# Kernel tuning notes

Hardware: AMD Instinct MI355X
Metric: run time of the kernel (lower is better)

Reference implementation:

```python
import jax, jax.numpy as jnp
import numpy as np

N = 50000   # total nodes
E = 100000  # total edges
F = 64      # input node features
H = 128     # hidden_dim
HEADS = 4
B = 64      # number of graphs in the batch
S = 512     # num_stations
LC = 8      # num_line_colors


def setup_inputs() -> dict:
    key = jax.random.key(0)
    ks = jax.random.split(key, 40)
    w = lambda i, shape: (jax.random.normal(ks[i], shape, jnp.float32) * 0.02)
    inp = {
        'node_features': jax.random.normal(ks[0], (N, F), jnp.float32),
        'edge_index': jax.random.randint(ks[1], (2, E), 0, N),
        'batch': jnp.sort(jax.random.randint(ks[2], (N,), 0, B)),
        # initial projection F -> H
        'Wp': w(3, (F, H)), 'bp': w(4, (H,)),
        # TransformerConv 1: in H, out H, heads HEADS (concat)
        'Wq1': w(5, (H, HEADS * H)), 'bq1': w(6, (HEADS * H,)),
        'Wk1': w(7, (H, HEADS * H)), 'bk1': w(8, (HEADS * H,)),
        'Wv1': w(9, (H, HEADS * H)), 'bv1': w(10, (HEADS * H,)),
        'Ws1': w(11, (H, HEADS * H)), 'bs1': w(12, (HEADS * H,)),
        # TransformerConv 2: in HEADS*H, out H, heads 1
        'Wq2': w(13, (HEADS * H, H)), 'bq2': w(14, (H,)),
        'Wk2': w(15, (HEADS * H, H)), 'bk2': w(16, (H,)),
        'Wv2': w(17, (HEADS * H, H)), 'bv2': w(18, (H,)),
        'Ws2': w(19, (HEADS * H, H)), 'bs2': w(20, (H,)),
        # output heads
        'crW': w(21, (H, 1)),  'crb': w(22, (1,)),
        'hlW': w(23, (H, 4)),  'hlb': w(24, (4,)),
        'mtW': w(25, (H, 3)),  'mtb': w(26, (3,)),
        'p1W': w(27, (H, S)),  'p1b': w(28, (S,)),
        'p2W': w(29, (H, S)),  'p2b': w(30, (S,)),
        'dtW': w(31, (H, S)),  'dtb': w(32, (S,)),
        'slW': w(33, (H, LC)), 'slb': w(34, (LC,)),
    }
    return inp


def transformer_conv(x, src, dst, Wq, bq, Wk, bk, Wv, bv, Ws, bs, heads, out_ch):
    # PyG TransformerConv (beta=False, concat=True, root_weight=True):
    #   alpha_ij = softmax_j( (W_q x_i) . (W_k x_j) / sqrt(d) ) over in-edges of i
    #   out_i    = sum_j alpha_ij * (W_v x_j)  (concat heads) + W_skip x_i
    n = x.shape[0]
    q = (x @ Wq + bq).reshape(n, heads, out_ch)
    k = (x @ Wk + bk).reshape(n, heads, out_ch)
    v = (x @ Wv + bv).reshape(n, heads, out_ch)
    scores = jnp.sum(q[dst] * k[src], axis=-1) / jnp.sqrt(jnp.float32(out_ch))  # [E,heads]
    m = jax.ops.segment_max(scores, dst, num_segments=n)                        # per-target max
    e = jnp.exp(scores - m[dst])
    denom = jax.ops.segment_sum(e, dst, num_segments=n)
    alpha = e / (denom[dst] + 1e-16)                                            # [E,heads]
    out = jax.ops.segment_sum(alpha[:, :, None] * v[src], dst, num_segments=n)  # [N,heads,out]
    return out.reshape(n, heads * out_ch) + (x @ Ws + bs)


def reference(node_features, edge_index, batch, Wp, bp,
              Wq1, bq1, Wk1, bk1, Wv1, bv1, Ws1, bs1,
              Wq2, bq2, Wk2, bk2, Wv2, bv2, Ws2, bs2,
              crW, crb, hlW, hlb, mtW, mtb, p1W, p1b, p2W, p2b, dtW, dtb, slW, slb):
    src, dst = edge_index[0], edge_index[1]
    h = jax.nn.relu(node_features @ Wp + bp)
    h = jax.nn.relu(transformer_conv(h, src, dst, Wq1, bq1, Wk1, bk1, Wv1, bv1, Ws1, bs1, HEADS, H))
    h = jax.nn.relu(transformer_conv(h, src, dst, Wq2, bq2, Wk2, bk2, Wv2, bv2, Ws2, bs2, 1, H))
    # global mean pool over graphs
    counts = jax.ops.segment_sum(jnp.ones((h.shape[0],), h.dtype), batch, num_segments=B)
    g = jax.ops.segment_sum(h, batch, num_segments=B) / jnp.maximum(counts, 1.0)[:, None]  # [B,H]
    value = g @ crW + crb
    return (value,
            g @ hlW + hlb,
            g @ mtW + mtb,
            g @ p1W + p1b,
            g @ p2W + p2b,
            g @ dtW + dtb,
            g @ slW + slb)
```

## Files before the change

kernel.cpp:

```cpp
#include <hip/hip_runtime.h>
#include <hip/hip_bf16.h>

#define NN 50000
#define EE 100000
#define FF 64
#define HH 128
#define HEADS 4
#define BB 64
#define SS 512
#define LCC 8

__device__ __forceinline__ float b2f(ushort u) {
    return __uint_as_float(((unsigned)u) << 16);
}
__device__ __forceinline__ ushort f2b(float f) {
    unsigned u = __float_as_uint(f);
    unsigned r = (u + 0x7FFFu + ((u >> 16) & 1u)) >> 16;
    return (ushort)r;
}
__device__ __forceinline__ uint f2b_pk(float a, float b) {
    __hip_bfloat162 h = __float22bfloat162_rn(make_float2(a, b));
    return *reinterpret_cast<uint*>(&h);
}

__device__ __forceinline__ uint f2fp8x4(float a, float b, float c, float d) {
    int r = __builtin_amdgcn_cvt_pk_fp8_f32(a, b, 0, false);
    r = __builtin_amdgcn_cvt_pk_fp8_f32(c, d, r, true);
    return (uint)r;
}
__device__ __forceinline__ float fp8lo(ushort u) { return __builtin_amdgcn_cvt_f32_fp8((int)u, 0); }
__device__ __forceinline__ float fp8hi(ushort u) { return __builtin_amdgcn_cvt_f32_fp8((int)u, 1); }

typedef __attribute__((ext_vector_type(4))) float f32x4;
typedef __attribute__((ext_vector_type(8))) short s16x8;
typedef __attribute__((ext_vector_type(4))) uint u32x4;

__device__ __forceinline__ void glls16(const ushort* g, ushort* l) {
    __builtin_amdgcn_global_load_lds((const __attribute__((address_space(1))) void*)g,
                                     (__attribute__((address_space(3))) void*)l, 16, 0, 0);
}

#define BM 128
#define BN 128
#define BK 64
#define EST 68

__global__ __launch_bounds__(256) void gemm_bf16(
    const ushort* __restrict__ A, const ushort* __restrict__ Bt,
    const float* __restrict__ bias,
    ushort* __restrict__ C1, int ld1,
    ushort* __restrict__ C2b, int mode,
    int M, int K, int relu, int gx, int gy)
{
    __shared__ __align__(16) ushort Sm[2 * BM * BK];
    ushort* As = Sm;
    ushort* Bs = Sm + BM * BK;

    const int bid  = blockIdx.x;
    const int xcd  = bid & 7;
    const int slot = bid >> 3;
    const int bx   = slot % gx;
    const int by   = xcd + 8 * (slot / gx);
    if (by >= gy) return;
    const int m0 = by * BM;
    const int n0 = bx * BN;

    const int t = threadIdx.x;
    const int lane = t & 63;
    const int wave = t >> 6;
    const int wm = (wave & 1) * 64;
    const int wn = (wave >> 1) * 64;
    const int lrow = lane & 15;
    const int g    = lane >> 4;

    const int wbase = n0 + wn;
    float bj[4];
#pragma unroll
    for (int j = 0; j < 4; ++j) bj[j] = bias[wbase + j * 16 + lrow];

    const int srow = (wave << 5) + (lane >> 3);
    const int scs  = lane & 7;

    const ushort* ga[4];
    const ushort* gb[4];
#pragma unroll
    for (int p = 0; p < 4; ++p) {
        const int row = srow + (p << 3);
        const int l   = scs ^ (row & 7);
        ga[p] = A + (size_t)min(m0 + row, M - 1) * K + (l << 3);
        gb[p] = Bt + (size_t)(n0 + row) * K + (l << 3);
    }
    const int ldsoff = (wave << 11);

    f32x4 acc[4][4];
#pragma unroll
    for (int i = 0; i < 4; ++i)
#pragma unroll
        for (int j = 0; j < 4; ++j)
            acc[i][j] = (f32x4){bj[j], bj[j], bj[j], bj[j]};

    for (int k0 = 0; k0 < K; k0 += BK) {
#pragma unroll
        for (int p = 0; p < 4; ++p) glls16(ga[p] + k0, As + ldsoff + (p << 9));
#pragma unroll
        for (int p = 0; p < 4; ++p) glls16(gb[p] + k0, Bs + ldsoff + (p << 9));
        __syncthreads();

#pragma unroll
        for (int kk = 0; kk < 2; ++kk) {
            s16x8 af[4], bf[4];
#pragma unroll
            for (int i = 0; i < 4; ++i) {
                const int R = wm + i * 16 + lrow;
                const int c = ((kk << 2) + g) ^ (R & 7);
                af[i] = *(const s16x8*)&As[(R << 6) + (c << 3)];
            }
#pragma unroll
            for (int j = 0; j < 4; ++j) {
                const int R = wn + j * 16 + lrow;
                const int c = ((kk << 2) + g) ^ (R & 7);
                bf[j] = *(const s16x8*)&Bs[(R << 6) + (c << 3)];
            }
#pragma unroll
            for (int i = 0; i < 4; ++i)
#pragma unroll
                for (int j = 0; j < 4; ++j)
                    acc[i][j] = __builtin_amdgcn_mfma_f32_16x16x32_bf16(af[i], bf[j], acc[i][j], 0, 0, 0);
        }
        __syncthreads();
    }

    float* Es = (float*)Sm + wave * (16 * EST);

    bool e8 = false;
    ushort* Cw = C1; int ldw = ld1; int cb = wbase;
    unsigned char* Cw8 = nullptr;
    if (mode == 1) {
        if (wbase >= 512) {
            e8 = true;
            const int u = wbase - 512;
            const int h = u >> 8;
            cb = u & 255;
            Cw8 = (unsigned char*)C2b + (size_t)h * NN * 256;
            ldw = 256;
        }
    } else if (mode == 2) {
        if (wbase < 128) { ldw = 128; }
        else {
            e8 = true;
            Cw8 = (unsigned char*)C2b;
            ldw = 384;
            cb = wbase - 128;
        }
    }

    const int rbase = (lane >> 4) * 4;
    const int rrow  = lane >> 2;
    const int rcol  = (lane & 3) << 4;

#pragma unroll
    for (int i = 0; i < 4; ++i) {
#pragma unroll
        for (int j = 0; j < 4; ++j)
#pragma unroll
            for (int r = 0; r < 4; ++r) {
                float v = acc[i][j][r];
                if (relu) v = fmaxf(v, 0.f);
                Es[(rbase + r) * EST + j * 16 + lrow] = v;
            }
        const int gm = m0 + wm + i * 16 + rrow;
        if (gm < M) {
            const float* srcp = Es + rrow * EST + rcol;
            f32x4 f0 = *(const f32x4*)(srcp + 0);
            f32x4 f1 = *(const f32x4*)(srcp + 4);
            f32x4 f2 = *(const f32x4*)(srcp + 8);
            f32x4 f3 = *(const f32x4*)(srcp + 12);
            if (!e8) {
                u32x4 o0, o1;
                o0[0] = f2b_pk(f0[0], f0[1]); o0[1] = f2b_pk(f0[2], f0[3]);
                o0[2] = f2b_pk(f1[0], f1[1]); o0[3] = f2b_pk(f1[2], f1[3]);
                o1[0] = f2b_pk(f2[0], f2[1]); o1[1] = f2b_pk(f2[2], f2[3]);
                o1[2] = f2b_pk(f3[0], f3[1]); o1[3] = f2b_pk(f3[2], f3[3]);
                ushort* dst = Cw + (size_t)gm * ldw + cb + rcol;
                *(u32x4*)(dst + 0) = o0;
                *(u32x4*)(dst + 8) = o1;
            } else {
                u32x4 o;
                o[0] = f2fp8x4(f0[0], f0[1], f0[2], f0[3]);
                o[1] = f2fp8x4(f1[0], f1[1], f1[2], f1[3]);
                o[2] = f2fp8x4(f2[0], f2[1], f2[2], f2[3]);
                o[3] = f2fp8x4(f3[0], f3[1], f3[2], f3[3]);
                *(u32x4*)(Cw8 + (size_t)gm * ldw + cb + rcol) = o;
            }
        }
    }
}

#define F1OFF  8192
#define F2OFF  204800
#define WTOTAL 466944
#define BTOT   2048
#define MWORK  (HEADS * 128 * 128 + HEADS * 128)

__global__ void prep_kernel(
    const float* __restrict__ Wp,
    const float* __restrict__ Wq1, const float* __restrict__ Wk1,
    const float* __restrict__ Wv1, const float* __restrict__ Ws1,
    const float* __restrict__ Wq2, const float* __restrict__ Wk2,
    const float* __restrict__ Wv2, const float* __restrict__ Ws2,
    const float* __restrict__ bs1, const float* __restrict__ bq1,
    const float* __restrict__ bv1, const float* __restrict__ bs2,
    const float* __restrict__ bq2, const float* __restrict__ bk2, const float* __restrict__ bv2,
    ushort* __restrict__ wt, float* __restrict__ bb)
{
    int t = blockIdx.x * 256 + threadIdx.x;
    if (t < WTOTAL) {
        float v;
        if (t < F1OFF) {
            int n = t >> 6, k = t & 63;
            v = Wp[k * 128 + n];
        } else if (t < F2OFF) {
            int u = t - F1OFF;
            int n = u >> 7, k = u & 127;
            if (n < 512) v = Ws1[k * 512 + n];
            else {
                int r = n - 512;
                int h = r >> 8, c = r & 255;
                if (c < 128) return;
                v = Wv1[k * 512 + h * 128 + (c - 128)] * 16.0f;
            }
        } else {
            int u = t - F2OFF;
            int n = u >> 9, k = u & 511;
            if (n < 128) v = Ws2[k * 128 + n];
            else {
                int r = n - 128;
                const float* W = (r < 128) ? Wq2 : (r < 256) ? Wk2 : Wv2;
                v = W[k * 128 + (r & 127)] * 16.0f;
            }
        }
        wt[t] = f2b(v);
    } else if (t < WTOTAL + BTOT) {
        int u = t - WTOTAL;
        float v;
        if (u < 512) v = bs1[u];
        else if (u < 1536) {
            int r = u - 512;
            int h = r >> 8, c = r & 255;
            if (c < 128) return;
            v = bv1[h * 128 + (c - 128)] * 16.0f;
        } else {
            int c = u - 1536;
            v = (c < 128) ? bs2[c]
              : (c < 256) ? bq2[c - 128] * 16.0f
              : (c < 384) ? bk2[c - 256] * 16.0f : bv2[c - 384] * 16.0f;
        }
        bb[u] = v;
    } else if (t < WTOTAL + BTOT + MWORK) {
        int m = t - (WTOTAL + BTOT);
        if (m < HEADS * 128 * 128) {
            int h = m >> 14;
            int rem = m & 16383;
            int b = rem >> 7, a = rem & 127;
            const float* wq = Wq1 + a * 512 + h * 128;
            const float* wk = Wk1 + b * 512 + h * 128;
            float acc = 0.f;
#pragma unroll 8
            for (int d = 0; d < 128; ++d) acc += wq[d] * wk[d];
            wt[F1OFF + (size_t)(512 + h * 256 + b) * 128 + a] = f2b(acc * 16.0f);
        } else {
            int u = m - HEADS * 128 * 128;
            int h = u >> 7, b = u & 127;
            const float* wk = Wk1 + b * 512 + h * 128;
            const float* bq = bq1 + h * 128;
            float acc = 0.f;
#pragma unroll 8
            for (int d = 0; d < 128; ++d) acc += wk[d] * bq[d];
            bb[512 + h * 256 + b] = acc * 16.0f;
        }
    }
}

__global__ void f32_to_bf16_kernel(const float4* __restrict__ in, uint2* __restrict__ out, int n4)
{
    int i = blockIdx.x * 256 + threadIdx.x;
    if (i >= n4) return;
    float4 v = in[i];
    uint2 o;
    o.x = f2b_pk(v.x, v.y);
    o.y = f2b_pk(v.z, v.w);
    out[i] = o;
}

__global__ void fill_kernel(unsigned* __restrict__ p, unsigned v, int n) {
    int i = blockIdx.x * blockDim.x + threadIdx.x;
    if (i < n) p[i] = v;
}

__global__ void hist_kernel(const int* __restrict__ dst, int* __restrict__ cnt, int E) {
    int e = blockIdx.x * 256 + threadIdx.x;
    if (e < E) atomicAdd(&cnt[dst[e]], 1);
}

#define SCAN_B 1024
__global__ void scan_bsum_kernel(const int* __restrict__ cnt, int* __restrict__ bsum, int n) {
    __shared__ int sd[256];
    int tid = threadIdx.x;
    int base = blockIdx.x * SCAN_B + tid * 4;
    int s = 0;
#pragma unroll
    for (int j = 0; j < 4; ++j) if (base + j < n) s += cnt[base + j];
    sd[tid] = s;
    __syncthreads();
    for (int off = 128; off > 0; off >>= 1) {
        if (tid < off) sd[tid] += sd[tid + off];
        __syncthreads();
    }
    if (tid == 0) bsum[blockIdx.x] = sd[0];
}

__global__ void scan_final_kernel(const int* __restrict__ cnt, const int* __restrict__ bsum,
                                  int* __restrict__ rowptr, int* __restrict__ cursor, int n) {
    __shared__ int sd[256];
    __shared__ int sb[256];
    int tid = threadIdx.x;
    sb[tid] = (tid < blockIdx.x) ? bsum[tid] : 0;
    __syncthreads();
    for (int off = 128; off > 0; off >>= 1) {
        if (tid < off) sb[tid] += sb[tid + off];
        __syncthreads();
    }
    const int bbase = sb[0];

    int base = blockIdx.x * SCAN_B + tid * 4;
    int v[4]; int s = 0;
#pragma unroll
    for (int j = 0; j < 4; ++j) { v[j] = (base + j < n) ? cnt[base + j] : 0; s += v[j]; }
    sd[tid] = s;
    __syncthreads();
    for (int off = 1; off < 256; off <<= 1) {
        int t2 = (tid >= off) ? sd[tid - off] : 0;
        __syncthreads();
        sd[tid] += t2;
        __syncthreads();
    }
    int acc = bbase + sd[tid] - s;
#pragma unroll
    for (int j = 0; j < 4; ++j) {
        if (base + j < n) cursor[base + j] = acc;
        acc += v[j];
        if (base + j < n) rowptr[base + j + 1] = acc;
    }
    if (blockIdx.x == 0 && tid == 0) rowptr[0] = 0;
}

__global__ void bucket_kernel(const int* __restrict__ src, const int* __restrict__ dst,
                              int* __restrict__ cursor, int* __restrict__ srcs, int E) {
    int e = blockIdx.x * 256 + threadIdx.x;
    if (e >= E) return;
    int p = atomicAdd(&cursor[dst[e]], 1);
    srcs[p] = src[e];
}

__global__ __launch_bounds__(256) void gather4_kernel(
    const unsigned char* __restrict__ Qb, const ushort* __restrict__ Kb,
    const int* __restrict__ rowptr, const int* __restrict__ srcs,
    ushort* __restrict__ io, float scale, int n)
{
    int i = blockIdx.x * 4 + (threadIdx.x >> 6);
    int lane = threadIdx.x & 63;
    if (i >= n) return;
    const ushort* Qu = (const ushort*)Qb;
    const uint* Ku = (const uint*)Kb;

    float q0[4], q1[4];
#pragma unroll
    for (int h = 0; h < 4; ++h) {
        ushort qv = Qu[((size_t)h * NN + i) * 128 + lane];
        q0[h] = fp8lo(qv); q1[h] = fp8hi(qv);
    }
    int p0 = rowptr[i], p1 = rowptr[i + 1];
    float den[4] = {0.f, 0.f, 0.f, 0.f};
    float o0[4] = {0.f, 0.f, 0.f, 0.f};
    float o1[4] = {0.f, 0.f, 0.f, 0.f};
    int p = p0;
    for (; p + 2 <= p1; p += 2) {
        int s0 = srcs[p], s1 = srcs[p + 1];
        uint kva = Ku[(size_t)s0 * 64 + lane];
        uint kvb = Ku[(size_t)s1 * 64 + lane];
        ushort vva[4], vvb[4];
#pragma unroll
        for (int h = 0; h < 4; ++h) vva[h] = Qu[((size_t)h * NN + s0) * 128 + 64 + lane];
#pragma unroll
        for (int h = 0; h < 4; ++h) vvb[h] = Qu[((size_t)h * NN + s1) * 128 + 64 + lane];
        float ka0 = b2f((ushort)kva), ka1 = b2f((ushort)(kva >> 16));
        float kb0 = b2f((ushort)kvb), kb1 = b2f((ushort)(kvb >> 16));
        float da[4], db[4];
#pragma unroll
        for (int h = 0; h < 4; ++h) {
            da[h] = q0[h] * ka0 + q1[h] * ka1;
            db[h] = q0[h] * kb0 + q1[h] * kb1;
        }
#pragma unroll
        for (int off = 32; off > 0; off >>= 1) {
#pragma unroll
            for (int h = 0; h < 4; ++h) {
                da[h] += __shfl_xor(da[h], off, 64);
                db[h] += __shfl_xor(db[h], off, 64);
            }
        }
#pragma unroll
        for (int h = 0; h < 4; ++h) {
            float ea = __expf(da[h] * scale);
            float eb = __expf(db[h] * scale);
            den[h] += ea + eb;
            o0[h] += ea * fp8lo(vva[h]) + eb * fp8lo(vvb[h]);
            o1[h] += ea * fp8hi(vva[h]) + eb * fp8hi(vvb[h]);
        }
    }
    if (p < p1) {
        int s = srcs[p];
        uint kv = Ku[(size_t)s * 64 + lane];
        ushort vv[4];
#pragma unroll
        for (int h = 0; h < 4; ++h) vv[h] = Qu[((size_t)h * NN + s) * 128 + 64 + lane];
        float k0 = b2f((ushort)kv), k1 = b2f((ushort)(kv >> 16));
        float d[4];
#pragma unroll
        for (int h = 0; h < 4; ++h) d[h] = q0[h] * k0 + q1[h] * k1;
#pragma unroll
        for (int off = 32; off > 0; off >>= 1) {
#pragma unroll
            for (int h = 0; h < 4; ++h) d[h] += __shfl_xor(d[h], off, 64);
        }
#pragma unroll
        for (int h = 0; h < 4; ++h) {
            float e = __expf(d[h] * scale);
            den[h] += e;
            o0[h] += e * fp8lo(vv[h]);
            o1[h] += e * fp8hi(vv[h]);
        }
    }
#pragma unroll
    for (int h = 0; h < 4; ++h) {
        uint sk = ((const uint*)io)[(size_t)i * 256 + h * 64 + lane];
        float inv = 0.0625f / (den[h] + 1e-16f);
        float r0 = fmaxf(b2f((ushort)sk) + o0[h] * inv, 0.f);
        float r1 = fmaxf(b2f((ushort)(sk >> 16)) + o1[h] * inv, 0.f);
        ((uint*)io)[(size_t)i * 256 + h * 64 + lane] = f2b_pk(r0, r1);
    }
}

__global__ __launch_bounds__(256) void edge_gather_kernel(
    const unsigned char* __restrict__ qkv,
    const int* __restrict__ rowptr, const int* __restrict__ srcs,
    const ushort* __restrict__ skip,
    ushort* __restrict__ outp, float scale, int n)
{
    int i = blockIdx.x * 4 + (threadIdx.x >> 6);
    int lane = threadIdx.x & 63;
    if (i >= n) return;
    const ushort* Qu = (const ushort*)qkv;

    uint sk = ((const uint*)skip)[(size_t)i * 64 + lane];
    ushort qv = Qu[(size_t)i * 192 + lane];
    float q0 = fp8lo(qv), q1 = fp8hi(qv);
    int p0 = rowptr[i], p1 = rowptr[i + 1];
    float den = 0.f, o0 = 0.f, o1 = 0.f;
    int p = p0;
    for (; p + 2 <= p1; p += 2) {
        int s0 = srcs[p], s1 = srcs[p + 1];
        const ushort* kr0 = Qu + (size_t)s0 * 192 + 64;
        const ushort* kr1 = Qu + (size_t)s1 * 192 + 64;
        ushort kv0 = kr0[lane], vv0 = kr0[lane + 64];
        ushort kv1 = kr1[lane], vv1 = kr1[lane + 64];
        float d0 = q0 * fp8lo(kv0) + q1 * fp8hi(kv0);
        float d1 = q0 * fp8lo(kv1) + q1 * fp8hi(kv1);
#pragma unroll
        for (int off = 32; off > 0; off >>= 1) {
            d0 += __shfl_xor(d0, off, 64);
            d1 += __shfl_xor(d1, off, 64);
        }
        float e0 = __expf(d0 * scale), e1 = __expf(d1 * scale);
        den += e0 + e1;
        o0 += e0 * fp8lo(vv0) + e1 * fp8lo(vv1);
        o1 += e0 * fp8hi(vv0) + e1 * fp8hi(vv1);
    }
    if (p < p1) {
        int s = srcs[p];
        const ushort* kr = Qu + (size_t)s * 192 + 64;
        ushort kv = kr[lane], vv = kr[lane + 64];
        float d = q0 * fp8lo(kv) + q1 * fp8hi(kv);
#pragma unroll
        for (int off = 32; off > 0; off >>= 1) d += __shfl_xor(d, off, 64);
        float e = __expf(d * scale);
        den += e;
        o0 += e * fp8lo(vv);
        o1 += e * fp8hi(vv);
    }
    float inv = 0.0625f / (den + 1e-16f);
    float r0 = b2f((ushort)sk) + o0 * inv;
    float r1 = b2f((ushort)(sk >> 16)) + o1 * inv;
    ((uint*)outp)[(size_t)i * 64 + lane] = f2b_pk(r0, r1);
}

__global__ __launch_bounds__(256) void pool_kernel(
    const ushort* __restrict__ h, const int* __restrict__ batch,
    float* __restrict__ gsum, float* __restrict__ cnt, int n)
{
    int wave = threadIdx.x >> 6, lane = threadIdx.x & 63;
    int start = blockIdx.x * 256 + wave * 64;
    int end = min(start + 64, n);
    if (start >= end) return;
    int cur = batch[start];
    float a0 = 0.f, a1 = 0.f;
    int run = 0;
    for (int node = start; node < end; ++node) {
        int g = batch[node];
        if (g != cur) {
            atomicAdd(&gsum[cur * HH + 2 * lane], a0);
            atomicAdd(&gsum[cur * HH + 2 * lane + 1], a1);
            if (lane == 0) atomicAdd(&cnt[cur], (float)run);
            cur = g; a0 = a1 = 0.f; run = 0;
        }
        uint x = ((const uint*)h)[(size_t)node * 64 + lane];
        a0 += fmaxf(b2f((ushort)x), 0.f);
        a1 += fmaxf(b2f((ushort)(x >> 16)), 0.f);
        ++run;
    }
    atomicAdd(&gsum[cur * HH + 2 * lane], a0);
    atomicAdd(&gsum[cur * HH + 2 * lane + 1], a1);
    if (lane == 0) atomicAdd(&cnt[cur], (float)run);
}

__global__ void pool_fin_kernel(const float* __restrict__ gsum,
                                const float* __restrict__ cnt, float* __restrict__ g)
{
    int i = blockIdx.x * blockDim.x + threadIdx.x;
    if (i < BB * HH) g[i] = gsum[i] / fmaxf(cnt[i / HH], 1.0f);
}

__global__ void out_heads_kernel(
    const float* __restrict__ g,
    const float* __restrict__ w0, const float* __restrict__ b0,
    const float* __restrict__ w1, const float* __restrict__ b1,
    const float* __restrict__ w2, const float* __restrict__ b2,
    const float* __restrict__ w3, const float* __restrict__ b3,
    const float* __restrict__ w4, const float* __restrict__ b4,
    const float* __restrict__ w5, const float* __restrict__ b5,
    const float* __restrict__ w6, const float* __restrict__ b6,
    float* __restrict__ out, int total)
{
    int t = blockIdx.x * blockDim.x + threadIdx.x;
    if (t >= total) return;
    const float* W; const float* bias; int cols; int local;
    if      (t < 64)    { W = w0; bias = b0; cols = 1;   local = t; }
    else if (t < 320)   { W = w1; bias = b1; cols = 4;   local = t - 64; }
    else if (t < 512)   { W = w2; bias = b2; cols = 3;   local = t - 320; }
    else if (t < 33280) { W = w3; bias = b3; cols = SS;  local = t - 512; }
    else if (t < 66048) { W = w4; bias = b4; cols = SS;  local = t - 33280; }
    else if (t < 98816) { W = w5; bias = b5; cols = SS;  local = t - 66048; }
    else                { W = w6; bias = b6; cols = LCC; local = t - 98816; }
    int b = local / cols, c = local % cols;
    const float* gr = g + b * HH;
    float acc = bias[c];
#pragma unroll 8
    for (int i = 0; i < HH; ++i) acc += gr[i] * W[i * cols + c];
    out[t] = acc;
}

extern "C" void kernel_launch(void* const* d_in, const int* in_sizes, int n_in,
                              void* d_out, int out_size, void* d_ws, size_t ws_size,
                              hipStream_t stream)
{
    (void)in_sizes; (void)n_in; (void)out_size; (void)ws_size;

    const float* nf   = (const float*)d_in[0];
    const int*   ei   = (const int*)d_in[1];
    const int*   src  = ei;
    const int*   dst  = ei + EE;
    const int*   batch= (const int*)d_in[2];
    const float* Wp   = (const float*)d_in[3];
    const float* bp   = (const float*)d_in[4];
    const float* Wq1  = (const float*)d_in[5];
    const float* bq1  = (const float*)d_in[6];
    const float* Wk1  = (const float*)d_in[7];
    const float* bk1  = (const float*)d_in[8];
    const float* Wv1  = (const float*)d_in[9];
    const float* bv1  = (const float*)d_in[10];
    const float* Ws1  = (const float*)d_in[11];
    const float* bs1  = (const float*)d_in[12];
    const float* Wq2  = (const float*)d_in[13];
    const float* bq2  = (const float*)d_in[14];
    const float* Wk2  = (const float*)d_in[15];
    const float* bk2  = (const float*)d_in[16];
    const float* Wv2  = (const float*)d_in[17];
    const float* bv2  = (const float*)d_in[18];
    const float* Ws2  = (const float*)d_in[19];
    const float* bs2  = (const float*)d_in[20];
    const float* crW  = (const float*)d_in[21];
    const float* crb  = (const float*)d_in[22];
    const float* hlW  = (const float*)d_in[23];
    const float* hlb  = (const float*)d_in[24];
    const float* mtW  = (const float*)d_in[25];
    const float* mtb  = (const float*)d_in[26];
    const float* p1W  = (const float*)d_in[27];
    const float* p1b  = (const float*)d_in[28];
    const float* p2W  = (const float*)d_in[29];
    const float* p2b  = (const float*)d_in[30];
    const float* dtW  = (const float*)d_in[31];
    const float* dtb  = (const float*)d_in[32];
    const float* slW  = (const float*)d_in[33];
    const float* slb  = (const float*)d_in[34];
    float* out = (float*)d_out;

    (void)bk1;

    unsigned char* base = (unsigned char*)d_ws;
    unsigned char* Qb8  = base;
    ushort* nfb  = (ushort*)base;
    ushort* h2sb = (ushort*)base;
    unsigned char* qkv8 = base + (size_t)NN * 256;
    ushort* h2   = (ushort*)(base + (size_t)NN * 640);
    ushort* h0b  = (ushort*)(base + (size_t)NN * 1024);
    ushort* h1b  = (ushort*)(base + (size_t)NN * 1280);
    ushort* wt   = (ushort*)(base + (size_t)NN * 2304);
    float*  bb   = (float*)(wt + WTOTAL);
    int*    rowptr = (int*)(bb + BTOT);
    int*    srcs   = rowptr + NN + 1;
    int*    cnt    = srcs + EE;
    float*  gsum   = (float*)(cnt + NN);
    float*  cntb   = gsum + BB * HH;
    int*    cursor = (int*)(cntb + BB);
    int*    bsum   = cursor + NN;
    float*  gbuf   = (float*)(bsum + 64);

    const float scale = 0.08838834764831845f;
    const dim3 blk(256);
    const int gy  = (NN + BM - 1) / BM;
    const int gyp = ((gy + 7) / 8) * 8;
    const int nb = (NN + SCAN_B - 1) / SCAN_B;

    prep_kernel<<<(WTOTAL + BTOT + MWORK + 255) / 256, blk, 0, stream>>>(
        Wp, Wq1, Wk1, Wv1, Ws1, Wq2, Wk2, Wv2, Ws2,
        bs1, bq1, bv1, bs2, bq2, bk2, bv2, wt, bb);

    f32_to_bf16_kernel<<<((NN * FF / 4) + 255) / 256, blk, 0, stream>>>(
        (const float4*)nf, (uint2*)nfb, NN * FF / 4);

    fill_kernel<<<(NN + BB * HH + BB + 255) / 256, blk, 0, stream>>>(
        (unsigned*)cnt, 0u, NN + BB * HH + BB);
    hist_kernel<<<(EE + 255) / 256, blk, 0, stream>>>(dst, cnt, EE);
    scan_bsum_kernel<<<nb, blk, 0, stream>>>(cnt, bsum, NN);
    scan_final_kernel<<<nb, blk, 0, stream>>>(cnt, bsum, rowptr, cursor, NN);
    bucket_kernel<<<(EE + 255) / 256, blk, 0, stream>>>(src, dst, cursor, srcs, EE);

    gemm_bf16<<<dim3(1 * gyp), blk, 0, stream>>>(
        nfb, wt, bp, h0b, HH, h0b, 0, NN, FF, 1, 1, gy);

    gemm_bf16<<<dim3(12 * gyp), blk, 0, stream>>>(
        h0b, wt + F1OFF, bb, h1b, 512, (ushort*)Qb8, 1, NN, HH, 0, 12, gy);

    gather4_kernel<<<(NN + 3) / 4, blk, 0, stream>>>(
        Qb8, h0b, rowptr, srcs, h1b, scale * 0.0625f, NN);

    gemm_bf16<<<dim3(4 * gyp), blk, 0, stream>>>(
        h1b, wt + F2OFF, bb + 1536, h2sb, 128, (ushort*)qkv8, 2, NN, 4 * HH, 0, 4, gy);

    edge_gather_kernel<<<(NN + 3) / 4, blk, 0, stream>>>(
        qkv8, rowptr, srcs, h2sb, h2, scale * 0.00390625f, NN);

    pool_kernel<<<(NN + 255) / 256, blk, 0, stream>>>(h2, batch, gsum, cntb, NN);
    pool_fin_kernel<<<(BB * HH + 255) / 256, blk, 0, stream>>>(gsum, cntb, gbuf);

    const int total = BB * (1 + 4 + 3 + SS + SS + SS + LCC);
    out_heads_kernel<<<(total + 255) / 256, blk, 0, stream>>>(
        gbuf, crW, crb, hlW, hlb, mtW, mtb, p1W, p1b, p2W, p2b, dtW, dtb, slW, slb, out, total);
}
```

Baseline: 339.6 us.

## Store layer-1 skip in fp8, vectorize gather kernels by head, fuse fill

```diff
diff --git a/kernel.cpp b/kernel.cpp
--- a/kernel.cpp
+++ b/kernel.cpp
@@ -28,8 +28,11 @@
     r = __builtin_amdgcn_cvt_pk_fp8_f32(c, d, r, true);
     return (uint)r;
 }
-__device__ __forceinline__ float fp8lo(ushort u) { return __builtin_amdgcn_cvt_f32_fp8((int)u, 0); }
-__device__ __forceinline__ float fp8hi(ushort u) { return __builtin_amdgcn_cvt_f32_fp8((int)u, 1); }
+__device__ __forceinline__ void fp8x4(uint u, float* f) {
+    auto lo = __builtin_amdgcn_cvt_pk_f32_fp8((int)u, false);
+    auto hi = __builtin_amdgcn_cvt_pk_f32_fp8((int)u, true);
+    f[0] = lo[0]; f[1] = lo[1]; f[2] = hi[0]; f[3] = hi[1];
+}
 
 typedef __attribute__((ext_vector_type(4))) float f32x4;
 typedef __attribute__((ext_vector_type(8))) short s16x8;
@@ -136,8 +139,11 @@
     ushort* Cw = C1; int ldw = ld1; int cb = wbase;
     unsigned char* Cw8 = nullptr;
     if (mode == 1) {
-        if (wbase >= 512) {
-            e8 = true;
+        e8 = true;
+        if (wbase < 512) {
+            Cw8 = (unsigned char*)C1;
+            ldw = 512;
+        } else {
             const int u = wbase - 512;
             const int h = u >> 8;
             cb = u & 255;
@@ -222,7 +228,7 @@
         } else if (t < F2OFF) {
             int u = t - F1OFF;
             int n = u >> 7, k = u & 127;
-            if (n < 512) v = Ws1[k * 512 + n];
+            if (n < 512) v = Ws1[k * 512 + n] * 16.0f;
             else {
                 int r = n - 512;
                 int h = r >> 8, c = r & 255;
@@ -243,7 +249,7 @@
     } else if (t < WTOTAL + BTOT) {
         int u = t - WTOTAL;
         float v;
-        if (u < 512) v = bs1[u];
+        if (u < 512) v = bs1[u] * 16.0f;
         else if (u < 1536) {
             int r = u - 512;
             int h = r >> 8, c = r & 255;
@@ -281,20 +287,20 @@
     }
 }
 
-__global__ void f32_to_bf16_kernel(const float4* __restrict__ in, uint2* __restrict__ out, int n4)
+__global__ void cvt_fill_kernel(const float4* __restrict__ in, uint2* __restrict__ out, int n4,
+                                unsigned* __restrict__ fillp, int filln)
 {
     int i = blockIdx.x * 256 + threadIdx.x;
-    if (i >= n4) return;
-    float4 v = in[i];
-    uint2 o;
-    o.x = f2b_pk(v.x, v.y);
-    o.y = f2b_pk(v.z, v.w);
-    out[i] = o;
-}
-
-__global__ void fill_kernel(unsigned* __restrict__ p, unsigned v, int n) {
-    int i = blockIdx.x * blockDim.x + threadIdx.x;
-    if (i < n) p[i] = v;
+    if (i < n4) {
+        float4 v = in[i];
+        uint2 o;
+        o.x = f2b_pk(v.x, v.y);
+        o.y = f2b_pk(v.z, v.w);
+        out[i] = o;
+    } else {
+        int j = i - n4;
+        if (j < filln) fillp[j] = 0u;
+    }
 }
 
 __global__ void hist_kernel(const int* __restrict__ dst, int* __restrict__ cnt, int E) {
@@ -365,90 +371,80 @@
 __global__ __launch_bounds__(256) void gather4_kernel(
     const unsigned char* __restrict__ Qb, const ushort* __restrict__ Kb,
     const int* __restrict__ rowptr, const int* __restrict__ srcs,
-    ushort* __restrict__ io, float scale, int n)
+    const unsigned char* __restrict__ s8,
+    ushort* __restrict__ outp, float scale, int n)
 {
     int i = blockIdx.x * 4 + (threadIdx.x >> 6);
     int lane = threadIdx.x & 63;
     if (i >= n) return;
-    const ushort* Qu = (const ushort*)Qb;
-    const uint* Ku = (const uint*)Kb;
-
-    float q0[4], q1[4];
-#pragma unroll
-    for (int h = 0; h < 4; ++h) {
-        ushort qv = Qu[((size_t)h * NN + i) * 128 + lane];
-        q0[h] = fp8lo(qv); q1[h] = fp8hi(qv);
-    }
+    const int h = lane >> 4;
+    const int l = lane & 15;
+
+    const unsigned char* Qh = Qb + (size_t)h * ((size_t)NN * 256);
+
+    uint2 uq = *(const uint2*)(Qh + (size_t)i * 256 + l * 8);
+    float q[8];
+    fp8x4(uq.x, q); fp8x4(uq.y, q + 4);
+
     int p0 = rowptr[i], p1 = rowptr[i + 1];
-    float den[4] = {0.f, 0.f, 0.f, 0.f};
-    float o0[4] = {0.f, 0.f, 0.f, 0.f};
-    float o1[4] = {0.f, 0.f, 0.f, 0.f};
+    float den = 0.f;
+    float o[8] = {0.f, 0.f, 0.f, 0.f, 0.f, 0.f, 0.f, 0.f};
     int p = p0;
     for (; p + 2 <= p1; p += 2) {
         int s0 = srcs[p], s1 = srcs[p + 1];
-        uint kva = Ku[(size_t)s0 * 64 + lane];
-        uint kvb = Ku[(size_t)s1 * 64 + lane];
-        ushort vva[4], vvb[4];
-#pragma unroll
-        for (int h = 0; h < 4; ++h) vva[h] = Qu[((size_t)h * NN + s0) * 128 + 64 + lane];
-#pragma unroll
-        for (int h = 0; h < 4; ++h) vvb[h] = Qu[((size_t)h * NN + s1) * 128 + 64 + lane];
-        float ka0 = b2f((ushort)kva), ka1 = b2f((ushort)(kva >> 16));
-        float kb0 = b2f((ushort)kvb), kb1 = b2f((ushort)(kvb >> 16));
-        float da[4], db[4];
-#pragma unroll
-        for (int h = 0; h < 4; ++h) {
-            da[h] = q0[h] * ka0 + q1[h] * ka1;
-            db[h] = q0[h] * kb0 + q1[h] * kb1;
-        }
-#pragma unroll
-        for (int off = 32; off > 0; off >>= 1) {
-#pragma unroll
-            for (int h = 0; h < 4; ++h) {
-                da[h] += __shfl_xor(da[h], off, 64);
-                db[h] += __shfl_xor(db[h], off, 64);
-            }
-        }
-#pragma unroll
-        for (int h = 0; h < 4; ++h) {
-            float ea = __expf(da[h] * scale);
-            float eb = __expf(db[h] * scale);
-            den[h] += ea + eb;
-            o0[h] += ea * fp8lo(vva[h]) + eb * fp8lo(vvb[h]);
-            o1[h] += ea * fp8hi(vva[h]) + eb * fp8hi(vvb[h]);
-        }
+        s16x8 ka = *(const s16x8*)(Kb + (size_t)s0 * 128 + l * 8);
+        s16x8 kb = *(const s16x8*)(Kb + (size_t)s1 * 128 + l * 8);
+        uint2 va = *(const uint2*)(Qh + (size_t)s0 * 256 + 128 + l * 8);
+        uint2 vb = *(const uint2*)(Qh + (size_t)s1 * 256 + 128 + l * 8);
+        float da = 0.f, db = 0.f;
+#pragma unroll
+        for (int d = 0; d < 8; ++d) {
+            da += q[d] * b2f((ushort)ka[d]);
+            db += q[d] * b2f((ushort)kb[d]);
+        }
+#pragma unroll
+        for (int off = 8; off > 0; off >>= 1) {
+            da += __shfl_xor(da, off, 64);
+            db += __shfl_xor(db, off, 64);
+        }
+        float ea = __expf(da * scale);
+        float eb = __expf(db * scale);
+        den += ea + eb;
+        float fa[8], fb[8];
+        fp8x4(va.x, fa); fp8x4(va.y, fa + 4);
+        fp8x4(vb.x, fb); fp8x4(vb.y, fb + 4);
+#pragma unroll
+        for (int d = 0; d < 8; ++d) o[d] += ea * fa[d] + eb * fb[d];
     }
     if (p < p1) {
         int s = srcs[p];
-        uint kv = Ku[(size_t)s * 64 + lane];
-        ushort vv[4];
-#pragma unroll
-        for (int h = 0; h < 4; ++h) vv[h] = Qu[((size_t)h * NN + s) * 128 + 64 + lane];
-        float k0 = b2f((ushort)kv), k1 = b2f((ushort)(kv >> 16));
-        float d[4];
-#pragma unroll
-        for (int h = 0; h < 4; ++h) d[h] = q0[h] * k0 + q1[h] * k1;
-#pragma unroll
-        for (int off = 32; off > 0; off >>= 1) {
-#pragma unroll
-            for (int h = 0; h < 4; ++h) d[h] += __shfl_xor(d[h], off, 64);
-        }
-#pragma unroll
-        for (int h = 0; h < 4; ++h) {
-            float e = __expf(d[h] * scale);
-            den[h] += e;
-            o0[h] += e * fp8lo(vv[h]);
-            o1[h] += e * fp8hi(vv[h]);
-        }
-    }
-#pragma unroll
-    for (int h = 0; h < 4; ++h) {
-        uint sk = ((const uint*)io)[(size_t)i * 256 + h * 64 + lane];
-        float inv = 0.0625f / (den[h] + 1e-16f);
-        float r0 = fmaxf(b2f((ushort)sk) + o0[h] * inv, 0.f);
-        float r1 = fmaxf(b2f((ushort)(sk >> 16)) + o1[h] * inv, 0.f);
-        ((uint*)io)[(size_t)i * 256 + h * 64 + lane] = f2b_pk(r0, r1);
-    }
+        s16x8 kv = *(const s16x8*)(Kb + (size_t)s * 128 + l * 8);
+        uint2 vv = *(const uint2*)(Qh + (size_t)s * 256 + 128 + l * 8);
+        float d0 = 0.f;
+#pragma unroll
+        for (int d = 0; d < 8; ++d) d0 += q[d] * b2f((ushort)kv[d]);
+#pragma unroll
+        for (int off = 8; off > 0; off >>= 1) d0 += __shfl_xor(d0, off, 64);
+        float e = __expf(d0 * scale);
+        den += e;
+        float fv[8];
+        fp8x4(vv.x, fv); fp8x4(vv.y, fv + 4);
+#pragma unroll
+        for (int d = 0; d < 8; ++d) o[d] += e * fv[d];
+    }
+    float invd = 1.0f / (den + 1e-16f);
+    uint2 sk = *(const uint2*)(s8 + (size_t)i * 512 + h * 128 + l * 8);
+    float skf[8];
+    fp8x4(sk.x, skf); fp8x4(sk.y, skf + 4);
+    float r[8];
+#pragma unroll
+    for (int d = 0; d < 8; ++d) r[d] = 0.0625f * fmaxf(skf[d] + o[d] * invd, 0.f);
+    u32x4 ov;
+    ov[0] = f2b_pk(r[0], r[1]);
+    ov[1] = f2b_pk(r[2], r[3]);
+    ov[2] = f2b_pk(r[4], r[5]);
+    ov[3] = f2b_pk(r[6], r[7]);
+    *(u32x4*)(outp + (size_t)i * 512 + h * 128 + l * 8) = ov;
 }
 
 __global__ __launch_bounds__(256) void edge_gather_kernel(
@@ -460,48 +456,56 @@
     int i = blockIdx.x * 4 + (threadIdx.x >> 6);
     int lane = threadIdx.x & 63;
     if (i >= n) return;
-    const ushort* Qu = (const ushort*)qkv;
-
-    uint sk = ((const uint*)skip)[(size_t)i * 64 + lane];
-    ushort qv = Qu[(size_t)i * 192 + lane];
-    float q0 = fp8lo(qv), q1 = fp8hi(qv);
+    const int g = lane >> 4;
+    const int l = lane & 15;
+
+    uint2 uq = *(const uint2*)(qkv + (size_t)i * 384 + l * 8);
+    float q[8];
+    fp8x4(uq.x, q); fp8x4(uq.y, q + 4);
+
     int p0 = rowptr[i], p1 = rowptr[i + 1];
-    float den = 0.f, o0 = 0.f, o1 = 0.f;
-    int p = p0;
-    for (; p + 2 <= p1; p += 2) {
-        int s0 = srcs[p], s1 = srcs[p + 1];
-        const ushort* kr0 = Qu + (size_t)s0 * 192 + 64;
-        const ushort* kr1 = Qu + (size_t)s1 * 192 + 64;
-        ushort kv0 = kr0[lane], vv0 = kr0[lane + 64];
-        ushort kv1 = kr1[lane], vv1 = kr1[lane + 64];
-        float d0 = q0 * fp8lo(kv0) + q1 * fp8hi(kv0);
-        float d1 = q0 * fp8lo(kv1) + q1 * fp8hi(kv1);
-#pragma unroll
-        for (int off = 32; off > 0; off >>= 1) {
-            d0 += __shfl_xor(d0, off, 64);
-            d1 += __shfl_xor(d1, off, 64);
-        }
-        float e0 = __expf(d0 * scale), e1 = __expf(d1 * scale);
-        den += e0 + e1;
-        o0 += e0 * fp8lo(vv0) + e1 * fp8lo(vv1);
-        o1 += e0 * fp8hi(vv0) + e1 * fp8hi(vv1);
-    }
-    if (p < p1) {
-        int s = srcs[p];
-        const ushort* kr = Qu + (size_t)s * 192 + 64;
-        ushort kv = kr[lane], vv = kr[lane + 64];
-        float d = q0 * fp8lo(kv) + q1 * fp8hi(kv);
-#pragma unroll
-        for (int off = 32; off > 0; off >>= 1) d += __shfl_xor(d, off, 64);
-        float e = __expf(d * scale);
+    float den = 0.f;
+    float o[8] = {0.f, 0.f, 0.f, 0.f, 0.f, 0.f, 0.f, 0.f};
+    for (int pb = p0; pb < p1; pb += 4) {
+        int p = pb + g;
+        bool act = p < p1;
+        int s = srcs[act ? p : p0];
+        const unsigned char* row = qkv + (size_t)s * 384;
+        uint2 kv = *(const uint2*)(row + 128 + l * 8);
+        uint2 vv = *(const uint2*)(row + 256 + l * 8);
+        float kf[8];
+        fp8x4(kv.x, kf); fp8x4(kv.y, kf + 4);
+        float d0 = 0.f;
+#pragma unroll
+        for (int d = 0; d < 8; ++d) d0 += q[d] * kf[d];
+#pragma unroll
+        for (int off = 8; off > 0; off >>= 1) d0 += __shfl_xor(d0, off, 64);
+        float e = act ? __expf(d0 * scale) : 0.f;
         den += e;
-        o0 += e * fp8lo(vv);
-        o1 += e * fp8hi(vv);
-    }
-    float inv = 0.0625f / (den + 1e-16f);
-    float r0 = b2f((ushort)sk) + o0 * inv;
-    float r1 = b2f((ushort)(sk >> 16)) + o1 * inv;
-    ((uint*)outp)[(size_t)i * 64 + lane] = f2b_pk(r0, r1);
+        float vf[8];
+        fp8x4(vv.x, vf); fp8x4(vv.y, vf + 4);
+#pragma unroll
+        for (int d = 0; d < 8; ++d) o[d] += e * vf[d];
+    }
+#pragma unroll
+    for (int off = 16; off < 64; off <<= 1) {
+        den += __shfl_xor(den, off, 64);
+#pragma unroll
+        for (int d = 0; d < 8; ++d) o[d] += __shfl_xor(o[d], off, 64);
+    }
+    if (g == 0) {
+        float inv = 0.0625f / (den + 1e-16f);
+        s16x8 sk = *(const s16x8*)(skip + (size_t)i * 128 + l * 8);
+        float r[8];
+#pragma unroll
+        for (int d = 0; d < 8; ++d) r[d] = b2f((ushort)sk[d]) + o[d] * inv;
+        u32x4 ov;
+        ov[0] = f2b_pk(r[0], r[1]);
+        ov[1] = f2b_pk(r[2], r[3]);
+        ov[2] = f2b_pk(r[4], r[5]);
+        ov[3] = f2b_pk(r[6], r[7]);
+        *(u32x4*)(outp + (size_t)i * 128 + l * 8) = ov;
+    }
 }
 
 __global__ __launch_bounds__(256) void pool_kernel(
@@ -624,7 +628,8 @@
     ushort* h2   = (ushort*)(base + (size_t)NN * 640);
     ushort* h0b  = (ushort*)(base + (size_t)NN * 1024);
     ushort* h1b  = (ushort*)(base + (size_t)NN * 1280);
-    ushort* wt   = (ushort*)(base + (size_t)NN * 2304);
+    unsigned char* s8 = base + (size_t)NN * 2304;
+    ushort* wt   = (ushort*)(base + (size_t)NN * 2816);
     float*  bb   = (float*)(wt + WTOTAL);
     int*    rowptr = (int*)(bb + BTOT);
     int*    srcs   = rowptr + NN + 1;
@@ -645,11 +650,11 @@
         Wp, Wq1, Wk1, Wv1, Ws1, Wq2, Wk2, Wv2, Ws2,
         bs1, bq1, bv1, bs2, bq2, bk2, bv2, wt, bb);
 
-    f32_to_bf16_kernel<<<((NN * FF / 4) + 255) / 256, blk, 0, stream>>>(
-        (const float4*)nf, (uint2*)nfb, NN * FF / 4);
-
-    fill_kernel<<<(NN + BB * HH + BB + 255) / 256, blk, 0, stream>>>(
-        (unsigned*)cnt, 0u, NN + BB * HH + BB);
+    const int n4 = NN * FF / 4;
+    const int filln = NN + BB * HH + BB;
+    cvt_fill_kernel<<<(n4 + filln + 255) / 256, blk, 0, stream>>>(
+        (const float4*)nf, (uint2*)nfb, n4, (unsigned*)cnt, filln);
+
     hist_kernel<<<(EE + 255) / 256, blk, 0, stream>>>(dst, cnt, EE);
     scan_bsum_kernel<<<nb, blk, 0, stream>>>(cnt, bsum, NN);
     scan_final_kernel<<<nb, blk, 0, stream>>>(cnt, bsum, rowptr, cursor, NN);
@@ -659,10 +664,10 @@
         nfb, wt, bp, h0b, HH, h0b, 0, NN, FF, 1, 1, gy);
 
     gemm_bf16<<<dim3(12 * gyp), blk, 0, stream>>>(
-        h0b, wt + F1OFF, bb, h1b, 512, (ushort*)Qb8, 1, NN, HH, 0, 12, gy);
+        h0b, wt + F1OFF, bb, (ushort*)s8, 512, (ushort*)Qb8, 1, NN, HH, 0, 12, gy);
 
     gather4_kernel<<<(NN + 3) / 4, blk, 0, stream>>>(
-        Qb8, h0b, rowptr, srcs, h1b, scale * 0.0625f, NN);
+        Qb8, h0b, rowptr, srcs, s8, h1b, scale * 0.0625f, NN);
 
     gemm_bf16<<<dim3(4 * gyp), blk, 0, stream>>>(
         h1b, wt + F2OFF, bb + 1536, h2sb, 128, (ushort*)qkv8, 2, NN, 4 * HH, 0, 4, gy);
```

Result: faster. 330.5 us (-2.7%).
